# Kernel tuning notes

Measured on AMD Instinct MI355X. Metric: run time of the kernel, lower is better.

The kernel has to match this reference:

```python
import jax, jax.numpy as jnp
import numpy as np

N = 100000      # nodes
E = 1600000     # edges
G = 1024        # graphs in batch
BASE = 1000     # baseline (TF-IDF) dim
AUG = 384       # augmented (LM) dim
H = 256         # hidden dim
C = 2           # classes
EPS = 1e-5      # BatchNorm eps


def setup_inputs() -> dict:
    key = jax.random.key(0)
    ks = jax.random.split(key, 10)
    x = jax.random.normal(ks[0], (N, BASE), jnp.float32)
    x_aug = jax.random.normal(ks[1], (N, AUG), jnp.float32)
    edge_index = jax.random.randint(ks[2], (2, E), 0, N)
    batch = jnp.sort(jax.random.randint(ks[3], (N,), 0, G))

    def lin(k, fin, fout):
        return (jax.random.normal(k, (fin, fout), jnp.float32) / np.sqrt(fin)).astype(jnp.float32)

    return dict(
        x=x, x_aug=x_aug,
        fusion_W=lin(ks[4], BASE + AUG, H), fusion_b=jnp.zeros((H,), jnp.float32),
        W0=lin(ks[5], H, H), b0=jnp.zeros((H,), jnp.float32),
        g0=jnp.ones((H,), jnp.float32), be0=jnp.zeros((H,), jnp.float32),
        W1=lin(ks[6], H, H), b1=jnp.zeros((H,), jnp.float32),
        g1=jnp.ones((H,), jnp.float32), be1=jnp.zeros((H,), jnp.float32),
        fc_W=lin(ks[7], H, C), fc_b=jnp.zeros((C,), jnp.float32),
        edge_index=edge_index, batch=batch,
    )


def _gcn(h, W, b, src, dst, dinv):
    # PyG GCNConv: x' = D^{-1/2}(A+I)D^{-1/2} (x W) + b, self-loop weight 1
    h = h @ W                                     # [N, H]
    norm = dinv[src] * dinv[dst]                  # [E]
    agg = jax.ops.segment_sum(h[src] * norm[:, None], dst, num_segments=N)
    agg = agg + h * (dinv * dinv)[:, None]        # self-loop term
    return agg + b


def _bn(x, gamma, beta):
    # training-mode BatchNorm1d (batch statistics, biased variance)
    m = x.mean(axis=0)
    v = x.var(axis=0)
    return (x - m) * jax.lax.rsqrt(v + EPS) * gamma + beta


def reference(x, x_aug, fusion_W, fusion_b, W0, b0, g0, be0, W1, b1, g1, be1,
              fc_W, fc_b, edge_index, batch):
    src, dst = edge_index[0], edge_index[1]
    # degrees with self-loops (edge weight 1), scattered at destination
    deg = jnp.zeros((N,), x.dtype).at[dst].add(1.0) + 1.0
    dinv = jax.lax.rsqrt(deg)

    # feature fusion ('concat'): Linear(baseline+aug -> hidden) + ReLU
    h = jax.nn.relu(jnp.concatenate([x, x_aug], axis=1) @ fusion_W + fusion_b)

    # GCN layer 1 + BN + ReLU (dropout is identity in eval)
    h = jax.nn.relu(_bn(_gcn(h, W0, b0, src, dst, dinv), g0, be0))
    # GCN layer 2 + BN + ReLU
    h = jax.nn.relu(_bn(_gcn(h, W1, b1, src, dst, dinv), g1, be1))

    # global mean pool over graphs
    cnt = jax.ops.segment_sum(jnp.ones((N,), h.dtype), batch, num_segments=G)
    pooled = jax.ops.segment_sum(h, batch, num_segments=G) / jnp.maximum(cnt, 1.0)[:, None]

    logits = pooled @ fc_W + fc_b                 # [G, C]
    return jax.nn.log_softmax(logits, axis=1)
```

## Files before the change

kernel.cpp:

```cpp
#include <hip/hip_runtime.h>
#include <hip/hip_bf16.h>

#define N_NODES 100000
#define N_EDGES 1600000
#define N_GRAPH 1024
#define DIM_BASE 1000
#define DIM_AUG 384
#define DIM_IN 1384
#define KPAD_IN 1408
#define HD 256
#define BN_EPS 1e-5f

typedef _Float16 f16x8 __attribute__((ext_vector_type(8)));
typedef _Float16 f16x4 __attribute__((ext_vector_type(4)));
typedef float f32x4 __attribute__((ext_vector_type(4)));

__global__ void zero_kernel(unsigned int* __restrict__ p, int n) {
    int i = blockIdx.x * blockDim.x + threadIdx.x;
    if (i < n) p[i] = 0u;
}

__global__ void count_edges_kernel(const int* __restrict__ dst, int* __restrict__ counts, int e) {
    int i = blockIdx.x * blockDim.x + threadIdx.x;
    if (i < e) atomicAdd(&counts[dst[i]], 1);
}

__global__ __launch_bounds__(256) void deg_bsum_kernel(const int* __restrict__ counts,
                                                       int* __restrict__ bsum, int n) {
    __shared__ int sh[256];
    int t = threadIdx.x;
    int base = blockIdx.x * 1024 + t * 4;
    int s = 0;
    if (base < n) {
        int4 v = *(const int4*)&counts[base];
        s = v.x + v.y + v.z + v.w;
    }
    sh[t] = s;
    __syncthreads();
    for (int off = 128; off > 0; off >>= 1) {
        if (t < off) sh[t] += sh[t + off];
        __syncthreads();
    }
    if (t == 0) bsum[blockIdx.x] = sh[0];
}

__global__ __launch_bounds__(128) void scan_bsum_kernel(const int* __restrict__ bsum,
                                                        int* __restrict__ boff, int nb) {
    __shared__ int sh[128];
    int t = threadIdx.x;
    int v = (t < nb) ? bsum[t] : 0;
    sh[t] = v;
    __syncthreads();
    for (int off = 1; off < 128; off <<= 1) {
        int u = (t >= off) ? sh[t - off] : 0;
        __syncthreads();
        sh[t] += u;
        __syncthreads();
    }
    if (t < nb) boff[t] = sh[t] - v;
}

__global__ __launch_bounds__(256) void emit_csr_kernel(const int* __restrict__ counts,
                                                       const int* __restrict__ boff,
                                                       int* __restrict__ row_ptr,
                                                       int* __restrict__ cursor,
                                                       float* __restrict__ dinv, int n, int etot) {
    __shared__ int sh[256];
    int t = threadIdx.x;
    int base = blockIdx.x * 1024 + t * 4;
    int c0 = 0, c1 = 0, c2 = 0, c3 = 0;
    if (base < n) {
        int4 v = *(const int4*)&counts[base];
        c0 = v.x; c1 = v.y; c2 = v.z; c3 = v.w;
    }
    int s = c0 + c1 + c2 + c3;
    sh[t] = s;
    __syncthreads();
    for (int off = 1; off < 256; off <<= 1) {
        int u = (t >= off) ? sh[t - off] : 0;
        __syncthreads();
        sh[t] += u;
        __syncthreads();
    }
    if (base < n) {
        int run = boff[blockIdx.x] + sh[t] - s;
        int4 rp;
        rp.x = run; run += c0;
        rp.y = run; run += c1;
        rp.z = run; run += c2;
        rp.w = run;
        *(int4*)&row_ptr[base] = rp;
        *(int4*)&cursor[base] = rp;
        float4 dv;
        dv.x = rsqrtf((float)c0 + 1.0f);
        dv.y = rsqrtf((float)c1 + 1.0f);
        dv.z = rsqrtf((float)c2 + 1.0f);
        dv.w = rsqrtf((float)c3 + 1.0f);
        *(float4*)&dinv[base] = dv;
    }
    if (blockIdx.x == 0 && t == 0) row_ptr[n] = etot;
}

__global__ void fill_edges_kernel(const int* __restrict__ src, const int* __restrict__ dst,
                                  int* __restrict__ cursor, int* __restrict__ col, int e) {
    int i = blockIdx.x * blockDim.x + threadIdx.x;
    if (i < e) {
        int pos = atomicAdd(&cursor[dst[i]], 1);
        col[pos] = src[i];
    }
}

__global__ __launch_bounds__(256) void btrans_kernel(const float* __restrict__ W,
                                                     f16x8* __restrict__ Bt,
                                                     int K, int nchunks) {
    int idx = blockIdx.x * 256 + threadIdx.x;
    if (idx >= nchunks) return;
    int col = idx & 255;
    int kbase = (idx >> 8) * 8;
    f16x8 h;
#pragma unroll
    for (int j = 0; j < 8; ++j) {
        int k = kbase + j;
        float v = (k < K) ? W[(size_t)k * HD + col] : 0.f;
        h[j] = (_Float16)v;
    }
    Bt[idx] = h;
}

__global__ __launch_bounds__(512, 4) void fusion_mfma_kernel(
        const float* __restrict__ x, const float* __restrict__ xa,
        const f16x8* __restrict__ Bt, const float* __restrict__ bias,
        _Float16* __restrict__ C, int M) {
    __shared__ _Float16 Al[2][128 * 40];
    int tid = threadIdx.x;
    int lane = tid & 63;
    int wid = tid >> 6;
    int wr = wid >> 2, wc = wid & 3;
    int l16 = lane & 15, l4 = lane >> 4;
    int row0 = blockIdx.x * 128;

    f32x4 acc[4][4];
#pragma unroll
    for (int m = 0; m < 4; ++m)
#pragma unroll
        for (int n = 0; n < 4; ++n) acc[m][n] = (f32x4){0.f, 0.f, 0.f, 0.f};

    int arow = tid >> 2;
    int akq = (tid & 3) * 8;
    int ar = row0 + arow;
    int arc = (ar < M) ? ar : (M - 1);

    auto loadA = [&](int s, float* fv) {
        int kg = s * 32 + akq;
        if (kg < DIM_IN) {
            const float* sp = (kg < DIM_BASE) ? (x + (size_t)arc * DIM_BASE + kg)
                                              : (xa + (size_t)arc * DIM_AUG + (kg - DIM_BASE));
            float4 v0 = ((const float4*)sp)[0];
            float4 v1 = ((const float4*)sp)[1];
            fv[0] = v0.x; fv[1] = v0.y; fv[2] = v0.z; fv[3] = v0.w;
            fv[4] = v1.x; fv[5] = v1.y; fv[6] = v1.z; fv[7] = v1.w;
        } else {
#pragma unroll
            for (int j = 0; j < 8; ++j) fv[j] = 0.f;
        }
    };

    const int S = KPAD_IN / 32;
    float fv0[8], fv1[8];
    loadA(0, fv0);
    loadA(1, fv1);

    int bcol = wc * 64 + l16;

    auto iter = [&](int s, float* fv) {
        int buf = s & 1;
        f16x8 av;
#pragma unroll
        for (int j = 0; j < 8; ++j) av[j] = (_Float16)fv[j];
        *(f16x8*)&Al[buf][arow * 40 + akq] = av;
        if (s + 2 < S) loadA(s + 2, fv);
        __syncthreads();
        f16x8 bf[4];
#pragma unroll
        for (int n = 0; n < 4; ++n)
            bf[n] = Bt[(size_t)(s * 4 + l4) * 256 + bcol + n * 16];
#pragma unroll
        for (int m = 0; m < 4; ++m) {
            f16x8 af = *(const f16x8*)&Al[buf][(wr * 64 + m * 16 + l16) * 40 + l4 * 8];
#pragma unroll
            for (int n = 0; n < 4; ++n)
                acc[m][n] = __builtin_amdgcn_mfma_f32_16x16x32_f16(af, bf[n], acc[m][n], 0, 0, 0);
        }
    };

    for (int s = 0; s < S; s += 2) {
        iter(s, fv0);
        iter(s + 1, fv1);
    }

#pragma unroll
    for (int n = 0; n < 4; ++n) {
        int colF = wc * 64 + n * 16 + l16;
        float bc = bias[colF];
#pragma unroll
        for (int m = 0; m < 4; ++m) {
#pragma unroll
            for (int r = 0; r < 4; ++r) {
                int rowF = row0 + wr * 64 + m * 16 + l4 * 4 + r;
                if (rowF < M)
                    C[(size_t)rowF * HD + colF] = (_Float16)fmaxf(acc[m][n][r] + bc, 0.f);
            }
        }
    }
}

__global__ __launch_bounds__(512, 4) void hgemm_f16_kernel(
        const _Float16* __restrict__ A, const f16x8* __restrict__ Bt,
        _Float16* __restrict__ C, int M) {
    __shared__ _Float16 Al[2][128 * 40];
    int tid = threadIdx.x;
    int lane = tid & 63;
    int wid = tid >> 6;
    int wr = wid >> 2, wc = wid & 3;
    int l16 = lane & 15, l4 = lane >> 4;
    int row0 = blockIdx.x * 128;

    f32x4 acc[4][4];
#pragma unroll
    for (int m = 0; m < 4; ++m)
#pragma unroll
        for (int n = 0; n < 4; ++n) acc[m][n] = (f32x4){0.f, 0.f, 0.f, 0.f};

    int arow = tid >> 2;
    int akq = (tid & 3) * 8;
    int ar = row0 + arow;
    int arc = (ar < M) ? ar : (M - 1);
    int bcol = wc * 64 + l16;

    const int S = HD / 32;
    f16x8 av0 = *(const f16x8*)&A[(size_t)arc * HD + akq];
    f16x8 av1 = *(const f16x8*)&A[(size_t)arc * HD + 32 + akq];

    auto iter = [&](int s, f16x8& av) {
        int buf = s & 1;
        *(f16x8*)&Al[buf][arow * 40 + akq] = av;
        if (s + 2 < S) av = *(const f16x8*)&A[(size_t)arc * HD + (s + 2) * 32 + akq];
        __syncthreads();
        f16x8 bf[4];
#pragma unroll
        for (int n = 0; n < 4; ++n)
            bf[n] = Bt[(size_t)(s * 4 + l4) * 256 + bcol + n * 16];
#pragma unroll
        for (int m = 0; m < 4; ++m) {
            f16x8 af = *(const f16x8*)&Al[buf][(wr * 64 + m * 16 + l16) * 40 + l4 * 8];
#pragma unroll
            for (int n = 0; n < 4; ++n)
                acc[m][n] = __builtin_amdgcn_mfma_f32_16x16x32_f16(af, bf[n], acc[m][n], 0, 0, 0);
        }
    };

    for (int s = 0; s < S; s += 2) {
        iter(s, av0);
        iter(s + 1, av1);
    }

#pragma unroll
    for (int n = 0; n < 4; ++n) {
        int colF = wc * 64 + n * 16 + l16;
#pragma unroll
        for (int m = 0; m < 4; ++m) {
#pragma unroll
            for (int r = 0; r < 4; ++r) {
                int rowF = row0 + wr * 64 + m * 16 + l4 * 4 + r;
                if (rowF < M)
                    C[(size_t)rowF * HD + colF] = (_Float16)acc[m][n][r];
            }
        }
    }
}

__global__ __launch_bounds__(512, 4) void hgemm_bn_kernel(
        const float* __restrict__ A, const f16x8* __restrict__ Bt,
        const float* __restrict__ bnp, _Float16* __restrict__ C, int M) {
    __shared__ _Float16 Al[2][128 * 40];
    __shared__ float bns[512];
    int tid = threadIdx.x;
    int lane = tid & 63;
    int wid = tid >> 6;
    int wr = wid >> 2, wc = wid & 3;
    int l16 = lane & 15, l4 = lane >> 4;
    int row0 = blockIdx.x * 128;

    bns[tid] = bnp[tid];
    __syncthreads();

    f32x4 acc[4][4];
#pragma unroll
    for (int m = 0; m < 4; ++m)
#pragma unroll
        for (int n = 0; n < 4; ++n) acc[m][n] = (f32x4){0.f, 0.f, 0.f, 0.f};

    int arow = tid >> 2;
    int akq = (tid & 3) * 8;
    int ar = row0 + arow;
    int arc = (ar < M) ? ar : (M - 1);
    int bcol = wc * 64 + l16;

    auto loadA = [&](int s, float* fv) {
        const float* sp = A + (size_t)arc * HD + s * 32 + akq;
        float4 v0 = ((const float4*)sp)[0];
        float4 v1 = ((const float4*)sp)[1];
        fv[0] = v0.x; fv[1] = v0.y; fv[2] = v0.z; fv[3] = v0.w;
        fv[4] = v1.x; fv[5] = v1.y; fv[6] = v1.z; fv[7] = v1.w;
    };

    const int S = HD / 32;
    float fv0[8], fv1[8];
    loadA(0, fv0);
    loadA(1, fv1);

    auto iter = [&](int s, float* fv) {
        int buf = s & 1;
        int kg = s * 32 + akq;
        f16x8 av;
#pragma unroll
        for (int j = 0; j < 8; ++j)
            av[j] = (_Float16)fmaxf(fmaf(fv[j], bns[kg + j], bns[HD + kg + j]), 0.f);
        *(f16x8*)&Al[buf][arow * 40 + akq] = av;
        if (s + 2 < S) loadA(s + 2, fv);
        __syncthreads();
        f16x8 bf[4];
#pragma unroll
        for (int n = 0; n < 4; ++n)
            bf[n] = Bt[(size_t)(s * 4 + l4) * 256 + bcol + n * 16];
#pragma unroll
        for (int m = 0; m < 4; ++m) {
            f16x8 af = *(const f16x8*)&Al[buf][(wr * 64 + m * 16 + l16) * 40 + l4 * 8];
#pragma unroll
            for (int n = 0; n < 4; ++n)
                acc[m][n] = __builtin_amdgcn_mfma_f32_16x16x32_f16(af, bf[n], acc[m][n], 0, 0, 0);
        }
    };

    for (int s = 0; s < S; s += 2) {
        iter(s, fv0);
        iter(s + 1, fv1);
    }

#pragma unroll
    for (int n = 0; n < 4; ++n) {
        int colF = wc * 64 + n * 16 + l16;
#pragma unroll
        for (int m = 0; m < 4; ++m) {
#pragma unroll
            for (int r = 0; r < 4; ++r) {
                int rowF = row0 + wr * 64 + m * 16 + l4 * 4 + r;
                if (rowF < M)
                    C[(size_t)rowF * HD + colF] = (_Float16)acc[m][n][r];
            }
        }
    }
}

__global__ __launch_bounds__(256) void agg_kernel(
        const _Float16* __restrict__ t, const float* __restrict__ dinv,
        const int* __restrict__ row_ptr, const int* __restrict__ col,
        const float* __restrict__ bias, float* __restrict__ outp, int n) {
    int wid = threadIdx.x >> 6;
    int lane = threadIdx.x & 63;
    int i = blockIdx.x * 4 + wid;
    if (i >= n) return;
    int c0 = lane * 4;
    float di = dinv[i];
    float di2 = di * di;
    f16x4 sv = *(const f16x4*)&t[(size_t)i * HD + c0];
    float a0 = (float)sv[0] * di2, a1 = (float)sv[1] * di2;
    float a2 = (float)sv[2] * di2, a3 = (float)sv[3] * di2;
    int e = row_ptr[i], end = row_ptr[i + 1];
    for (; e + 1 < end; e += 2) {
        int s0 = col[e], s1 = col[e + 1];
        float w0 = dinv[s0] * di, w1 = dinv[s1] * di;
        f16x4 v0 = *(const f16x4*)&t[(size_t)s0 * HD + c0];
        f16x4 v1 = *(const f16x4*)&t[(size_t)s1 * HD + c0];
        a0 = fmaf((float)v0[0], w0, a0); a1 = fmaf((float)v0[1], w0, a1);
        a2 = fmaf((float)v0[2], w0, a2); a3 = fmaf((float)v0[3], w0, a3);
        a0 = fmaf((float)v1[0], w1, a0); a1 = fmaf((float)v1[1], w1, a1);
        a2 = fmaf((float)v1[2], w1, a2); a3 = fmaf((float)v1[3], w1, a3);
    }
    if (e < end) {
        int s0 = col[e];
        float w0 = dinv[s0] * di;
        f16x4 v0 = *(const f16x4*)&t[(size_t)s0 * HD + c0];
        a0 = fmaf((float)v0[0], w0, a0); a1 = fmaf((float)v0[1], w0, a1);
        a2 = fmaf((float)v0[2], w0, a2); a3 = fmaf((float)v0[3], w0, a3);
    }
    float4 b = *(const float4*)&bias[c0];
    float4 o;
    o.x = a0 + b.x; o.y = a1 + b.y; o.z = a2 + b.z; o.w = a3 + b.w;
    *(float4*)&outp[(size_t)i * HD + c0] = o;
}

__global__ __launch_bounds__(256) void bn_stats_kernel(const float* __restrict__ a,
                                                       float* __restrict__ sums, int n) {
    int tid = threadIdx.x;
    int r0 = blockIdx.x * 256;
    int r1 = min(r0 + 256, n);
    float s = 0.f, s2 = 0.f;
    for (int r = r0; r < r1; ++r) {
        float v = a[(size_t)r * HD + tid];
        s += v;
        s2 = fmaf(v, v, s2);
    }
    atomicAdd(&sums[tid], s);
    atomicAdd(&sums[HD + tid], s2);
}

__global__ __launch_bounds__(256) void bn_final_kernel(const float* __restrict__ sums,
                                                       const float* __restrict__ g,
                                                       const float* __restrict__ be,
                                                       float* __restrict__ p, int n) {
    int tid = threadIdx.x;
    float mean = sums[tid] / (float)n;
    float var = sums[HD + tid] / (float)n - mean * mean;
    float sc = g[tid] * rsqrtf(var + BN_EPS);
    p[tid] = sc;
    p[HD + tid] = be[tid] - mean * sc;
}

__global__ void graph_cnt_kernel(const int* __restrict__ batch, float* __restrict__ cnt, int n) {
    int i = blockIdx.x * blockDim.x + threadIdx.x;
    if (i < n) atomicAdd(&cnt[batch[i]], 1.0f);
}

__global__ __launch_bounds__(256) void bn_relu_pool_kernel(const float* __restrict__ a,
                                                           const float* __restrict__ p,
                                                           const int* __restrict__ batch,
                                                           float* __restrict__ pooled, int n) {
    int tid = threadIdx.x;
    int n0 = blockIdx.x * 64;
    int n1 = min(n0 + 64, n);
    if (n0 >= n) return;
    float sc = p[tid], sh = p[HD + tid];
    int curg = batch[n0];
    float acc = 0.f;
    for (int i = n0; i < n1; ++i) {
        int g = batch[i];
        if (g != curg) {
            atomicAdd(&pooled[(size_t)curg * HD + tid], acc);
            acc = 0.f;
            curg = g;
        }
        acc += fmaxf(fmaf(a[(size_t)i * HD + tid], sc, sh), 0.f);
    }
    atomicAdd(&pooled[(size_t)curg * HD + tid], acc);
}

__global__ __launch_bounds__(64) void head_kernel(const float* __restrict__ pooled,
                                                  const float* __restrict__ cnt,
                                                  const float* __restrict__ fcW,
                                                  const float* __restrict__ fcb,
                                                  float* __restrict__ outp) {
    int g = blockIdx.x, lane = threadIdx.x;
    float inv = 1.0f / fmaxf(cnt[g], 1.0f);
    float a0 = 0.f, a1 = 0.f;
    for (int j = lane; j < HD; j += 64) {
        float v = pooled[(size_t)g * HD + j] * inv;
        a0 = fmaf(v, fcW[j * 2 + 0], a0);
        a1 = fmaf(v, fcW[j * 2 + 1], a1);
    }
    for (int off = 32; off > 0; off >>= 1) {
        a0 += __shfl_down(a0, off);
        a1 += __shfl_down(a1, off);
    }
    if (lane == 0) {
        float l0 = a0 + fcb[0], l1 = a1 + fcb[1];
        float m = fmaxf(l0, l1);
        float lse = m + logf(expf(l0 - m) + expf(l1 - m));
        outp[g * 2 + 0] = l0 - lse;
        outp[g * 2 + 1] = l1 - lse;
    }
}

extern "C" void kernel_launch(void* const* d_in, const int* in_sizes, int n_in,
                              void* d_out, int out_size, void* d_ws, size_t ws_size,
                              hipStream_t stream) {
    const float* x        = (const float*)d_in[0];
    const float* x_aug    = (const float*)d_in[1];
    const float* fusion_W = (const float*)d_in[2];
    const float* fusion_b = (const float*)d_in[3];
    const float* W0       = (const float*)d_in[4];
    const float* b0       = (const float*)d_in[5];
    const float* g0       = (const float*)d_in[6];
    const float* be0      = (const float*)d_in[7];
    const float* W1       = (const float*)d_in[8];
    const float* b1       = (const float*)d_in[9];
    const float* g1       = (const float*)d_in[10];
    const float* be1      = (const float*)d_in[11];
    const float* fc_W     = (const float*)d_in[12];
    const float* fc_b     = (const float*)d_in[13];
    const int*   eidx     = (const int*)d_in[14];
    const int*   batch    = (const int*)d_in[15];
    float* outp = (float*)d_out;

    const int N = N_NODES, E = N_EDGES, G = N_GRAPH;
    const int* src = eidx;
    const int* dst = eidx + E;

    size_t off = 0;
    char* ws = (char*)d_ws;
    auto take = [&](size_t nbytes) -> void* {
        void* p = ws + off;
        off = (off + nbytes + 255) & ~(size_t)255;
        return p;
    };
    float*     bufA    = (float*)take((size_t)N * HD * 4);
    _Float16*  bufH    = (_Float16*)take((size_t)N * HD * 2);
    _Float16*  bufT    = (_Float16*)take((size_t)N * HD * 2);
    float*     dinv    = (float*)take((size_t)N * 4);
    int*       row_ptr = (int*)take((size_t)(N + 1) * 4);
    int*       cursor  = (int*)take((size_t)N * 4);
    int*       col     = (int*)take((size_t)E * 4);
    float*     bn1p    = (float*)take(512 * 4);
    float*     bn2p    = (float*)take(512 * 4);
    int*       bsum    = (int*)take(128 * 4);
    int*       boff    = (int*)take(128 * 4);
    f16x8*     BtF     = (f16x8*)take((size_t)(KPAD_IN / 8) * 256 * 16);
    f16x8*     Bt0     = (f16x8*)take((size_t)(HD / 8) * 256 * 16);
    f16x8*     Bt1     = (f16x8*)take((size_t)(HD / 8) * 256 * 16);
    size_t zwords = (size_t)N + 512 + 512 + (size_t)G * HD + G;
    unsigned int* zbase = (unsigned int*)take(zwords * 4);
    int*   counts = (int*)zbase;
    float* bn1s   = (float*)(zbase + N);
    float* bn2s   = bn1s + 512;
    float* pooled = bn2s + 512;
    float* cnt    = pooled + (size_t)G * HD;

    const int nchF = (KPAD_IN / 8) * 256;
    const int nchH = (HD / 8) * 256;
    const int nScanB = (N + 1023) / 1024;

    zero_kernel<<<(int)((zwords + 255) / 256), 256, 0, stream>>>(zbase, (int)zwords);
    count_edges_kernel<<<(E + 255) / 256, 256, 0, stream>>>(dst, counts, E);
    deg_bsum_kernel<<<nScanB, 256, 0, stream>>>(counts, bsum, N);
    scan_bsum_kernel<<<1, 128, 0, stream>>>(bsum, boff, nScanB);
    emit_csr_kernel<<<nScanB, 256, 0, stream>>>(counts, boff, row_ptr, cursor, dinv, N, E);
    fill_edges_kernel<<<(E + 255) / 256, 256, 0, stream>>>(src, dst, cursor, col, E);
    btrans_kernel<<<(nchF + 255) / 256, 256, 0, stream>>>(fusion_W, BtF, DIM_IN, nchF);
    btrans_kernel<<<(nchH + 255) / 256, 256, 0, stream>>>(W0, Bt0, HD, nchH);
    btrans_kernel<<<(nchH + 255) / 256, 256, 0, stream>>>(W1, Bt1, HD, nchH);

    const int gblocks = (N + 127) / 128;
    fusion_mfma_kernel<<<gblocks, 512, 0, stream>>>(x, x_aug, BtF, fusion_b, bufH, N);
    hgemm_f16_kernel<<<gblocks, 512, 0, stream>>>(bufH, Bt0, bufT, N);
    agg_kernel<<<(N + 3) / 4, 256, 0, stream>>>(bufT, dinv, row_ptr, col, b0, bufA, N);
    bn_stats_kernel<<<(N + 255) / 256, 256, 0, stream>>>(bufA, bn1s, N);
    bn_final_kernel<<<1, 256, 0, stream>>>(bn1s, g0, be0, bn1p, N);
    hgemm_bn_kernel<<<gblocks, 512, 0, stream>>>(bufA, Bt1, bn1p, bufT, N);
    agg_kernel<<<(N + 3) / 4, 256, 0, stream>>>(bufT, dinv, row_ptr, col, b1, bufA, N);
    bn_stats_kernel<<<(N + 255) / 256, 256, 0, stream>>>(bufA, bn2s, N);
    bn_final_kernel<<<1, 256, 0, stream>>>(bn2s, g1, be1, bn2p, N);
    graph_cnt_kernel<<<(N + 255) / 256, 256, 0, stream>>>(batch, cnt, N);
    bn_relu_pool_kernel<<<(N + 63) / 64, 256, 0, stream>>>(bufA, bn2p, batch, pooled, N);
    head_kernel<<<G, 64, 0, stream>>>(pooled, cnt, fc_W, fc_b, outp);
}
```

Measured before the change: 1.017 ms.

## Restructure GEMMs to 32-row tiles with full-K swizzled LDS staging

```diff
diff --git a/kernel.cpp b/kernel.cpp
--- a/kernel.cpp
+++ b/kernel.cpp
@@ -14,6 +14,12 @@
 typedef _Float16 f16x8 __attribute__((ext_vector_type(8)));
 typedef _Float16 f16x4 __attribute__((ext_vector_type(4)));
 typedef float f32x4 __attribute__((ext_vector_type(4)));
+
+__device__ __forceinline__ void barrier_keep_vmem() {
+    __builtin_amdgcn_sched_barrier(0);
+    asm volatile("s_waitcnt lgkmcnt(0)\n\ts_barrier" ::: "memory");
+    __builtin_amdgcn_sched_barrier(0);
+}
 
 __global__ void zero_kernel(unsigned int* __restrict__ p, int n) {
     int i = blockIdx.x * blockDim.x + threadIdx.x;
@@ -127,238 +133,189 @@
     Bt[idx] = h;
 }
 
-__global__ __launch_bounds__(512, 4) void fusion_mfma_kernel(
+
+__global__ __launch_bounds__(1024, 4) void fusion_v3_kernel(
         const float* __restrict__ x, const float* __restrict__ xa,
         const f16x8* __restrict__ Bt, const float* __restrict__ bias,
-        _Float16* __restrict__ C, int M) {
-    __shared__ _Float16 Al[2][128 * 40];
+        _Float16* __restrict__ C) {
+    __shared__ __align__(16) _Float16 Al[32 * KPAD_IN];
     int tid = threadIdx.x;
     int lane = tid & 63;
-    int wid = tid >> 6;
-    int wr = wid >> 2, wc = wid & 3;
+    int w = tid >> 6;
     int l16 = lane & 15, l4 = lane >> 4;
-    int row0 = blockIdx.x * 128;
-
-    f32x4 acc[4][4];
-#pragma unroll
-    for (int m = 0; m < 4; ++m)
-#pragma unroll
-        for (int n = 0; n < 4; ++n) acc[m][n] = (f32x4){0.f, 0.f, 0.f, 0.f};
-
-    int arow = tid >> 2;
-    int akq = (tid & 3) * 8;
-    int ar = row0 + arow;
-    int arc = (ar < M) ? ar : (M - 1);
-
-    auto loadA = [&](int s, float* fv) {
-        int kg = s * 32 + akq;
-        if (kg < DIM_IN) {
-            const float* sp = (kg < DIM_BASE) ? (x + (size_t)arc * DIM_BASE + kg)
-                                              : (xa + (size_t)arc * DIM_AUG + (kg - DIM_BASE));
-            float4 v0 = ((const float4*)sp)[0];
-            float4 v1 = ((const float4*)sp)[1];
-            fv[0] = v0.x; fv[1] = v0.y; fv[2] = v0.z; fv[3] = v0.w;
-            fv[4] = v1.x; fv[5] = v1.y; fv[6] = v1.z; fv[7] = v1.w;
-        } else {
-#pragma unroll
-            for (int j = 0; j < 8; ++j) fv[j] = 0.f;
+    int row0 = blockIdx.x * 32;
+    int colF = w * 16 + l16;
+
+    float4 a1[6], a2[6];
+    auto loadA = [&](int h, float4* fv) {
+#pragma unroll
+        for (int r = 0; r < 6; ++r) {
+            int idx = tid + r * 1024;
+            if (idx < 5632) {
+                int row = idx / 176;
+                int c4 = idx - row * 176;
+                int col = c4 * 4 + h * 704;
+                int arow = row0 + row;
+                if (col < DIM_BASE)
+                    fv[r] = *(const float4*)&x[(size_t)arow * DIM_BASE + col];
+                else if (col < DIM_IN)
+                    fv[r] = *(const float4*)&xa[(size_t)arow * DIM_AUG + (col - DIM_BASE)];
+                else
+                    fv[r] = make_float4(0.f, 0.f, 0.f, 0.f);
+            }
         }
     };
-
-    const int S = KPAD_IN / 32;
-    float fv0[8], fv1[8];
-    loadA(0, fv0);
-    loadA(1, fv1);
-
-    int bcol = wc * 64 + l16;
-
-    auto iter = [&](int s, float* fv) {
-        int buf = s & 1;
-        f16x8 av;
-#pragma unroll
-        for (int j = 0; j < 8; ++j) av[j] = (_Float16)fv[j];
-        *(f16x8*)&Al[buf][arow * 40 + akq] = av;
-        if (s + 2 < S) loadA(s + 2, fv);
-        __syncthreads();
-        f16x8 bf[4];
-#pragma unroll
-        for (int n = 0; n < 4; ++n)
-            bf[n] = Bt[(size_t)(s * 4 + l4) * 256 + bcol + n * 16];
-#pragma unroll
-        for (int m = 0; m < 4; ++m) {
-            f16x8 af = *(const f16x8*)&Al[buf][(wr * 64 + m * 16 + l16) * 40 + l4 * 8];
-#pragma unroll
-            for (int n = 0; n < 4; ++n)
-                acc[m][n] = __builtin_amdgcn_mfma_f32_16x16x32_f16(af, bf[n], acc[m][n], 0, 0, 0);
+    auto cvwr = [&](int h, const float4* fv) {
+#pragma unroll
+        for (int r = 0; r < 6; ++r) {
+            int idx = tid + r * 1024;
+            if (idx < 5632) {
+                int row = idx / 176;
+                int c4 = idx - row * 176;
+                int cb = (c4 * 8 + h * 1408) ^ ((row & 7) << 4);
+                f16x4 hv;
+                hv[0] = (_Float16)fv[r].x; hv[1] = (_Float16)fv[r].y;
+                hv[2] = (_Float16)fv[r].z; hv[3] = (_Float16)fv[r].w;
+                *(f16x4*)((char*)Al + (size_t)row * 2816 + cb) = hv;
+            }
         }
     };
 
-    for (int s = 0; s < S; s += 2) {
-        iter(s, fv0);
-        iter(s + 1, fv1);
-    }
-
-#pragma unroll
-    for (int n = 0; n < 4; ++n) {
-        int colF = wc * 64 + n * 16 + l16;
-        float bc = bias[colF];
-#pragma unroll
-        for (int m = 0; m < 4; ++m) {
-#pragma unroll
-            for (int r = 0; r < 4; ++r) {
-                int rowF = row0 + wr * 64 + m * 16 + l4 * 4 + r;
-                if (rowF < M)
-                    C[(size_t)rowF * HD + colF] = (_Float16)fmaxf(acc[m][n][r] + bc, 0.f);
-            }
-        }
-    }
-}
-
-__global__ __launch_bounds__(512, 4) void hgemm_f16_kernel(
+    f32x4 acc0 = (f32x4){0.f, 0.f, 0.f, 0.f};
+    f32x4 acc1 = (f32x4){0.f, 0.f, 0.f, 0.f};
+    int xorv = (l16 & 7) << 4;
+    auto kstep = [&](int t, f16x8 bq) {
+        int kb = t * 64 + l4 * 16;
+        const char* base = (const char*)Al;
+        f16x8 af0 = *(const f16x8*)(base + (size_t)l16 * 2816 + (kb ^ xorv));
+        f16x8 af1 = *(const f16x8*)(base + (size_t)(16 + l16) * 2816 + (kb ^ xorv));
+        acc0 = __builtin_amdgcn_mfma_f32_16x16x32_f16(af0, bq, acc0, 0, 0, 0);
+        acc1 = __builtin_amdgcn_mfma_f32_16x16x32_f16(af1, bq, acc1, 0, 0, 0);
+    };
+    auto loadBc = [&](int t) -> f16x8 {
+        return Bt[(size_t)(t * 4 + l4) * 256 + colF];
+    };
+
+    const int NT = KPAD_IN / 32;
+    loadA(0, a1);
+    loadA(1, a2);
+    cvwr(0, a1);
+    barrier_keep_vmem();
+
+    f16x8 bq = loadBc(0);
+    for (int t = 0; t < 22; ++t) {
+        f16x8 bn2 = (t + 1 < NT) ? loadBc(t + 1) : bq;
+        kstep(t, bq);
+        bq = bn2;
+    }
+
+    cvwr(1, a2);
+    barrier_keep_vmem();
+
+    bq = loadBc(22);
+    for (int t = 22; t < NT; ++t) {
+        f16x8 bn2 = (t + 1 < NT) ? loadBc(t + 1) : bq;
+        kstep(t, bq);
+        bq = bn2;
+    }
+
+    float bc = bias[colF];
+#pragma unroll
+    for (int r = 0; r < 4; ++r) {
+        int rowF = row0 + l4 * 4 + r;
+        C[(size_t)rowF * HD + colF] = (_Float16)fmaxf(acc0[r] + bc, 0.f);
+        C[(size_t)(rowF + 16) * HD + colF] = (_Float16)fmaxf(acc1[r] + bc, 0.f);
+    }
+}
+
+__global__ __launch_bounds__(1024) void hgemm_f16_v3_kernel(
         const _Float16* __restrict__ A, const f16x8* __restrict__ Bt,
-        _Float16* __restrict__ C, int M) {
-    __shared__ _Float16 Al[2][128 * 40];
+        _Float16* __restrict__ C) {
+    __shared__ __align__(16) _Float16 Al[32 * HD];
     int tid = threadIdx.x;
     int lane = tid & 63;
-    int wid = tid >> 6;
-    int wr = wid >> 2, wc = wid & 3;
+    int w = tid >> 6;
     int l16 = lane & 15, l4 = lane >> 4;
-    int row0 = blockIdx.x * 128;
-
-    f32x4 acc[4][4];
-#pragma unroll
-    for (int m = 0; m < 4; ++m)
-#pragma unroll
-        for (int n = 0; n < 4; ++n) acc[m][n] = (f32x4){0.f, 0.f, 0.f, 0.f};
-
-    int arow = tid >> 2;
-    int akq = (tid & 3) * 8;
-    int ar = row0 + arow;
-    int arc = (ar < M) ? ar : (M - 1);
-    int bcol = wc * 64 + l16;
-
-    const int S = HD / 32;
-    f16x8 av0 = *(const f16x8*)&A[(size_t)arc * HD + akq];
-    f16x8 av1 = *(const f16x8*)&A[(size_t)arc * HD + 32 + akq];
-
-    auto iter = [&](int s, f16x8& av) {
-        int buf = s & 1;
-        *(f16x8*)&Al[buf][arow * 40 + akq] = av;
-        if (s + 2 < S) av = *(const f16x8*)&A[(size_t)arc * HD + (s + 2) * 32 + akq];
-        __syncthreads();
-        f16x8 bf[4];
-#pragma unroll
-        for (int n = 0; n < 4; ++n)
-            bf[n] = Bt[(size_t)(s * 4 + l4) * 256 + bcol + n * 16];
-#pragma unroll
-        for (int m = 0; m < 4; ++m) {
-            f16x8 af = *(const f16x8*)&Al[buf][(wr * 64 + m * 16 + l16) * 40 + l4 * 8];
-#pragma unroll
-            for (int n = 0; n < 4; ++n)
-                acc[m][n] = __builtin_amdgcn_mfma_f32_16x16x32_f16(af, bf[n], acc[m][n], 0, 0, 0);
-        }
-    };
-
-    for (int s = 0; s < S; s += 2) {
-        iter(s, av0);
-        iter(s + 1, av1);
-    }
-
-#pragma unroll
-    for (int n = 0; n < 4; ++n) {
-        int colF = wc * 64 + n * 16 + l16;
-#pragma unroll
-        for (int m = 0; m < 4; ++m) {
-#pragma unroll
-            for (int r = 0; r < 4; ++r) {
-                int rowF = row0 + wr * 64 + m * 16 + l4 * 4 + r;
-                if (rowF < M)
-                    C[(size_t)rowF * HD + colF] = (_Float16)acc[m][n][r];
-            }
-        }
-    }
-}
-
-__global__ __launch_bounds__(512, 4) void hgemm_bn_kernel(
+    int row0 = blockIdx.x * 32;
+    int colF = w * 16 + l16;
+
+    int srow = tid >> 5;
+    int sc8 = (tid & 31) * 8;
+    f16x8 v = *(const f16x8*)&A[(size_t)(row0 + srow) * HD + sc8];
+    *(f16x8*)((char*)Al + (size_t)srow * 512 + ((sc8 * 2) ^ ((srow & 7) << 4))) = v;
+    __syncthreads();
+
+    f32x4 acc0 = (f32x4){0.f, 0.f, 0.f, 0.f};
+    f32x4 acc1 = (f32x4){0.f, 0.f, 0.f, 0.f};
+    int xorv = (l16 & 7) << 4;
+#pragma unroll
+    for (int t = 0; t < HD / 32; ++t) {
+        f16x8 bq = Bt[(size_t)(t * 4 + l4) * 256 + colF];
+        int kb = t * 64 + l4 * 16;
+        f16x8 af0 = *(const f16x8*)((const char*)Al + (size_t)l16 * 512 + (kb ^ xorv));
+        f16x8 af1 = *(const f16x8*)((const char*)Al + (size_t)(16 + l16) * 512 + (kb ^ xorv));
+        acc0 = __builtin_amdgcn_mfma_f32_16x16x32_f16(af0, bq, acc0, 0, 0, 0);
+        acc1 = __builtin_amdgcn_mfma_f32_16x16x32_f16(af1, bq, acc1, 0, 0, 0);
+    }
+
+#pragma unroll
+    for (int r = 0; r < 4; ++r) {
+        int rowF = row0 + l4 * 4 + r;
+        C[(size_t)rowF * HD + colF] = (_Float16)acc0[r];
+        C[(size_t)(rowF + 16) * HD + colF] = (_Float16)acc1[r];
+    }
+}
+
+__global__ __launch_bounds__(1024) void hgemm_bn_v3_kernel(
         const float* __restrict__ A, const f16x8* __restrict__ Bt,
-        const float* __restrict__ bnp, _Float16* __restrict__ C, int M) {
-    __shared__ _Float16 Al[2][128 * 40];
-    __shared__ float bns[512];
+        const float* __restrict__ bnp, _Float16* __restrict__ C) {
+    __shared__ __align__(16) _Float16 Al[32 * HD];
     int tid = threadIdx.x;
     int lane = tid & 63;
-    int wid = tid >> 6;
-    int wr = wid >> 2, wc = wid & 3;
+    int w = tid >> 6;
     int l16 = lane & 15, l4 = lane >> 4;
-    int row0 = blockIdx.x * 128;
-
-    bns[tid] = bnp[tid];
+    int row0 = blockIdx.x * 32;
+    int colF = w * 16 + l16;
+
+    int srow = tid >> 5;
+    int sc8 = (tid & 31) * 8;
+    const float* ap = A + (size_t)(row0 + srow) * HD + sc8;
+    float4 v0 = ((const float4*)ap)[0];
+    float4 v1 = ((const float4*)ap)[1];
+    float4 s0 = *(const float4*)&bnp[sc8];
+    float4 s1 = *(const float4*)&bnp[sc8 + 4];
+    float4 h0 = *(const float4*)&bnp[HD + sc8];
+    float4 h1 = *(const float4*)&bnp[HD + sc8 + 4];
+    f16x8 hv;
+    hv[0] = (_Float16)fmaxf(fmaf(v0.x, s0.x, h0.x), 0.f);
+    hv[1] = (_Float16)fmaxf(fmaf(v0.y, s0.y, h0.y), 0.f);
+    hv[2] = (_Float16)fmaxf(fmaf(v0.z, s0.z, h0.z), 0.f);
+    hv[3] = (_Float16)fmaxf(fmaf(v0.w, s0.w, h0.w), 0.f);
+    hv[4] = (_Float16)fmaxf(fmaf(v1.x, s1.x, h1.x), 0.f);
+    hv[5] = (_Float16)fmaxf(fmaf(v1.y, s1.y, h1.y), 0.f);
+    hv[6] = (_Float16)fmaxf(fmaf(v1.z, s1.z, h1.z), 0.f);
+    hv[7] = (_Float16)fmaxf(fmaf(v1.w, s1.w, h1.w), 0.f);
+    *(f16x8*)((char*)Al + (size_t)srow * 512 + ((sc8 * 2) ^ ((srow & 7) << 4))) = hv;
     __syncthreads();
 
-    f32x4 acc[4][4];
-#pragma unroll
-    for (int m = 0; m < 4; ++m)
-#pragma unroll
-        for (int n = 0; n < 4; ++n) acc[m][n] = (f32x4){0.f, 0.f, 0.f, 0.f};
-
-    int arow = tid >> 2;
-    int akq = (tid & 3) * 8;
-    int ar = row0 + arow;
-    int arc = (ar < M) ? ar : (M - 1);
-    int bcol = wc * 64 + l16;
-
-    auto loadA = [&](int s, float* fv) {
-        const float* sp = A + (size_t)arc * HD + s * 32 + akq;
-        float4 v0 = ((const float4*)sp)[0];
-        float4 v1 = ((const float4*)sp)[1];
-        fv[0] = v0.x; fv[1] = v0.y; fv[2] = v0.z; fv[3] = v0.w;
-        fv[4] = v1.x; fv[5] = v1.y; fv[6] = v1.z; fv[7] = v1.w;
-    };
-
-    const int S = HD / 32;
-    float fv0[8], fv1[8];
-    loadA(0, fv0);
-    loadA(1, fv1);
-
-    auto iter = [&](int s, float* fv) {
-        int buf = s & 1;
-        int kg = s * 32 + akq;
-        f16x8 av;
-#pragma unroll
-        for (int j = 0; j < 8; ++j)
-            av[j] = (_Float16)fmaxf(fmaf(fv[j], bns[kg + j], bns[HD + kg + j]), 0.f);
-        *(f16x8*)&Al[buf][arow * 40 + akq] = av;
-        if (s + 2 < S) loadA(s + 2, fv);
-        __syncthreads();
-        f16x8 bf[4];
-#pragma unroll
-        for (int n = 0; n < 4; ++n)
-            bf[n] = Bt[(size_t)(s * 4 + l4) * 256 + bcol + n * 16];
-#pragma unroll
-        for (int m = 0; m < 4; ++m) {
-            f16x8 af = *(const f16x8*)&Al[buf][(wr * 64 + m * 16 + l16) * 40 + l4 * 8];
-#pragma unroll
-            for (int n = 0; n < 4; ++n)
-                acc[m][n] = __builtin_amdgcn_mfma_f32_16x16x32_f16(af, bf[n], acc[m][n], 0, 0, 0);
-        }
-    };
-
-    for (int s = 0; s < S; s += 2) {
-        iter(s, fv0);
-        iter(s + 1, fv1);
-    }
-
-#pragma unroll
-    for (int n = 0; n < 4; ++n) {
-        int colF = wc * 64 + n * 16 + l16;
-#pragma unroll
-        for (int m = 0; m < 4; ++m) {
-#pragma unroll
-            for (int r = 0; r < 4; ++r) {
-                int rowF = row0 + wr * 64 + m * 16 + l4 * 4 + r;
-                if (rowF < M)
-                    C[(size_t)rowF * HD + colF] = (_Float16)acc[m][n][r];
-            }
-        }
+    f32x4 acc0 = (f32x4){0.f, 0.f, 0.f, 0.f};
+    f32x4 acc1 = (f32x4){0.f, 0.f, 0.f, 0.f};
+    int xorv = (l16 & 7) << 4;
+#pragma unroll
+    for (int t = 0; t < HD / 32; ++t) {
+        f16x8 bq = Bt[(size_t)(t * 4 + l4) * 256 + colF];
+        int kb = t * 64 + l4 * 16;
+        f16x8 af0 = *(const f16x8*)((const char*)Al + (size_t)l16 * 512 + (kb ^ xorv));
+        f16x8 af1 = *(const f16x8*)((const char*)Al + (size_t)(16 + l16) * 512 + (kb ^ xorv));
+        acc0 = __builtin_amdgcn_mfma_f32_16x16x32_f16(af0, bq, acc0, 0, 0, 0);
+        acc1 = __builtin_amdgcn_mfma_f32_16x16x32_f16(af1, bq, acc1, 0, 0, 0);
+    }
+
+#pragma unroll
+    for (int r = 0; r < 4; ++r) {
+        int rowF = row0 + l4 * 4 + r;
+        C[(size_t)rowF * HD + colF] = (_Float16)acc0[r];
+        C[(size_t)(rowF + 16) * HD + colF] = (_Float16)acc1[r];
     }
 }
 
@@ -377,17 +334,24 @@
     float a0 = (float)sv[0] * di2, a1 = (float)sv[1] * di2;
     float a2 = (float)sv[2] * di2, a3 = (float)sv[3] * di2;
     int e = row_ptr[i], end = row_ptr[i + 1];
-    for (; e + 1 < end; e += 2) {
-        int s0 = col[e], s1 = col[e + 1];
+    for (; e + 3 < end; e += 4) {
+        int s0 = col[e], s1 = col[e + 1], s2 = col[e + 2], s3 = col[e + 3];
         float w0 = dinv[s0] * di, w1 = dinv[s1] * di;
+        float w2 = dinv[s2] * di, w3 = dinv[s3] * di;
         f16x4 v0 = *(const f16x4*)&t[(size_t)s0 * HD + c0];
         f16x4 v1 = *(const f16x4*)&t[(size_t)s1 * HD + c0];
+        f16x4 v2 = *(const f16x4*)&t[(size_t)s2 * HD + c0];
+        f16x4 v3 = *(const f16x4*)&t[(size_t)s3 * HD + c0];
         a0 = fmaf((float)v0[0], w0, a0); a1 = fmaf((float)v0[1], w0, a1);
         a2 = fmaf((float)v0[2], w0, a2); a3 = fmaf((float)v0[3], w0, a3);
         a0 = fmaf((float)v1[0], w1, a0); a1 = fmaf((float)v1[1], w1, a1);
         a2 = fmaf((float)v1[2], w1, a2); a3 = fmaf((float)v1[3], w1, a3);
-    }
-    if (e < end) {
+        a0 = fmaf((float)v2[0], w2, a0); a1 = fmaf((float)v2[1], w2, a1);
+        a2 = fmaf((float)v2[2], w2, a2); a3 = fmaf((float)v2[3], w2, a3);
+        a0 = fmaf((float)v3[0], w3, a0); a1 = fmaf((float)v3[1], w3, a1);
+        a2 = fmaf((float)v3[2], w3, a2); a3 = fmaf((float)v3[3], w3, a3);
+    }
+    for (; e < end; ++e) {
         int s0 = col[e];
         float w0 = dinv[s0] * di;
         f16x4 v0 = *(const f16x4*)&t[(size_t)s0 * HD + c0];
@@ -549,13 +513,13 @@
     btrans_kernel<<<(nchH + 255) / 256, 256, 0, stream>>>(W0, Bt0, HD, nchH);
     btrans_kernel<<<(nchH + 255) / 256, 256, 0, stream>>>(W1, Bt1, HD, nchH);
 
-    const int gblocks = (N + 127) / 128;
-    fusion_mfma_kernel<<<gblocks, 512, 0, stream>>>(x, x_aug, BtF, fusion_b, bufH, N);
-    hgemm_f16_kernel<<<gblocks, 512, 0, stream>>>(bufH, Bt0, bufT, N);
+    const int gb32 = N / 32;
+    fusion_v3_kernel<<<gb32, 1024, 0, stream>>>(x, x_aug, BtF, fusion_b, bufH);
+    hgemm_f16_v3_kernel<<<gb32, 1024, 0, stream>>>(bufH, Bt0, bufT);
     agg_kernel<<<(N + 3) / 4, 256, 0, stream>>>(bufT, dinv, row_ptr, col, b0, bufA, N);
     bn_stats_kernel<<<(N + 255) / 256, 256, 0, stream>>>(bufA, bn1s, N);
     bn_final_kernel<<<1, 256, 0, stream>>>(bn1s, g0, be0, bn1p, N);
-    hgemm_bn_kernel<<<gblocks, 512, 0, stream>>>(bufA, Bt1, bn1p, bufT, N);
+    hgemm_bn_v3_kernel<<<gb32, 1024, 0, stream>>>(bufA, Bt1, bn1p, bufT);
     agg_kernel<<<(N + 3) / 4, 256, 0, stream>>>(bufT, dinv, row_ptr, col, b1, bufA, N);
     bn_stats_kernel<<<(N + 255) / 256, 256, 0, stream>>>(bufA, bn2s, N);
     bn_final_kernel<<<1, 256, 0, stream>>>(bn2s, g1, be1, bn2p, N);
```

Result: no change. 997.5 us (-1.9%).
